# Performance work log

Measured on AMD Instinct MI355X. Metric: run time of the kernel, lower is better.

Reference implementation:

```python
import jax, jax.numpy as jnp
import numpy as np

B, DIN, D, C = 8192, 1024, 768, 16384

def setup_inputs() -> dict:
    key = jax.random.key(0)
    k1, k2, k3 = jax.random.split(key, 3)
    x = jax.random.normal(k1, (B, DIN), dtype=jnp.float32)
    W = jax.random.normal(k2, (DIN, D), dtype=jnp.float32) * 0.02  # backbone final projection
    centroids = jax.random.normal(k3, (C, D), dtype=jnp.float32)
    return {"x": x, "W": W, "centroids": centroids}

def reference(x, W, centroids):
    # backbone embedding: [B, D]
    e = x @ W
    # -||e - c||^2 via algebraic expansion: ||e||^2 + ||c||^2 - 2 e.c
    # (same math as -((e[:,None]-centroids[None])**2).sum(-1), GEMM-formulated)
    e_sq = jnp.sum(e * e, axis=-1, keepdims=True)          # [B, 1]
    c_sq = jnp.sum(centroids * centroids, axis=-1)         # [C]
    cross = e @ centroids.T                                # [B, C]
    return -(e_sq + c_sq[None, :] - 2.0 * cross)           # [B, C]
```

## Files before the change

### kernel.cpp

```cpp
#include <hip/hip_runtime.h>
#include <hip/hip_bf16.h>
#include <cstdint>
#include <cstddef>

#define BB   8192
#define DIN  1024
#define DD   768
#define CC   16384

typedef __bf16 bf16x8 __attribute__((ext_vector_type(8)));
typedef __bf16 bf16x4 __attribute__((ext_vector_type(4)));
typedef float  floatx4 __attribute__((ext_vector_type(4)));

__device__ __forceinline__ void gload_lds16(const void* g, void* l) {
    __builtin_amdgcn_global_load_lds(
        (const __attribute__((address_space(1))) void*)g,
        (__attribute__((address_space(3))) void*)l,
        16, 0, 0);
}


__global__ __launch_bounds__(256) void f2b_kernel(const float4* __restrict__ in,
                                                  bf16x4* __restrict__ out) {
    size_t i = (size_t)blockIdx.x * 256 + threadIdx.x;
    float4 v = in[i];
    bf16x4 o;
    o.x = (__bf16)v.x; o.y = (__bf16)v.y; o.z = (__bf16)v.z; o.w = (__bf16)v.w;
    out[i] = o;
}

__global__ __launch_bounds__(256) void row_convert_sumsq_f32(const float* __restrict__ src,
                                                             __bf16* __restrict__ dst,
                                                             float* __restrict__ sq,
                                                             int Dd) {
    int row = blockIdx.x;
    int tid = threadIdx.x, lane = tid & 63, wave = tid >> 6;
    const float* s = src + (size_t)row * Dd;
    __bf16* d = dst + (size_t)row * Dd;
    float acc = 0.f;
    for (int j = tid; j < Dd; j += 256) {
        __bf16 b = (__bf16)s[j];
        d[j] = b;
        float f = (float)b;
        acc += f * f;
    }
    for (int off = 32; off > 0; off >>= 1) acc += __shfl_xor(acc, off, 64);
    __shared__ float red[4];
    if (lane == 0) red[wave] = acc;
    __syncthreads();
    if (tid == 0) sq[row] = red[0] + red[1] + red[2] + red[3];
}

__global__ __launch_bounds__(256) void row_sumsq_bf16(const __bf16* __restrict__ src,
                                                      float* __restrict__ sq,
                                                      int Dd) {
    int row = blockIdx.x;
    int tid = threadIdx.x, lane = tid & 63, wave = tid >> 6;
    const __bf16* s = src + (size_t)row * Dd;
    float acc = 0.f;
    for (int j = tid; j < Dd; j += 256) {
        float f = (float)s[j];
        acc += f * f;
    }
    for (int off = 32; off > 0; off >>= 1) acc += __shfl_xor(acc, off, 64);
    __shared__ float red[4];
    if (lane == 0) red[wave] = acc;
    __syncthreads();
    if (tid == 0) sq[row] = red[0] + red[1] + red[2] + red[3];
}

__global__ __launch_bounds__(256) void transpose_w(const float* __restrict__ W,
                                                   __bf16* __restrict__ Wt,
                                                   int K, int N) {
    __shared__ float tile[32][33];
    int bx = blockIdx.x * 32;
    int by = blockIdx.y * 32;
    int tx = threadIdx.x & 31, ty = threadIdx.x >> 5;
    for (int i = 0; i < 32; i += 8)
        tile[ty + i][tx] = W[(size_t)(by + ty + i) * N + bx + tx];
    __syncthreads();
    for (int i = 0; i < 32; i += 8)
        Wt[(size_t)(bx + ty + i) * K + by + tx] = (__bf16)tile[tx][ty + i];
}

template <int EPI>
__global__ __launch_bounds__(256) void gemm_bt(const __bf16* __restrict__ A,
                                               const __bf16* __restrict__ Bt,
                                               void* __restrict__ OutP,
                                               const float* __restrict__ esq,
                                               const float* __restrict__ csq,
                                               int M, int N, int K) {
    __shared__ __bf16 As[128 * 64];
    __shared__ __bf16 Bs[128 * 64];
    const int tid  = threadIdx.x;
    const int lane = tid & 63;
    const int wave = tid >> 6;
    const int bm = blockIdx.x * 128;
    const int bn = blockIdx.y * 128;

    floatx4 acc[4][4] = {};

    const int srow = lane >> 3;
    const int sk   = (lane & 7) * 8;

    const int wm   = (wave & 1) * 64;
    const int wn   = (wave >> 1) * 64;
    const int frow = lane & 15;
    const int fk   = (lane >> 4) * 8;

    for (int k0 = 0; k0 < K; k0 += 64) {
        __syncthreads();
        #pragma unroll
        for (int i = 0; i < 4; ++i) {
            int row = wave * 32 + i * 8;
            const __bf16* ga = A  + (size_t)(bm + row + srow) * K + k0 + sk;
            gload_lds16(ga, &As[(size_t)row * 64]);
            const __bf16* gb = Bt + (size_t)(bn + row + srow) * K + k0 + sk;
            gload_lds16(gb, &Bs[(size_t)row * 64]);
        }
        asm volatile("s_waitcnt vmcnt(0)" ::: "memory");
        __syncthreads();

        #pragma unroll
        for (int kk = 0; kk < 64; kk += 32) {
            bf16x8 af[4], bfr[4];
            #pragma unroll
            for (int mi = 0; mi < 4; ++mi)
                af[mi] = *(const bf16x8*)&As[(wm + mi * 16 + frow) * 64 + kk + fk];
            #pragma unroll
            for (int ni = 0; ni < 4; ++ni)
                bfr[ni] = *(const bf16x8*)&Bs[(wn + ni * 16 + frow) * 64 + kk + fk];
            #pragma unroll
            for (int mi = 0; mi < 4; ++mi)
                #pragma unroll
                for (int ni = 0; ni < 4; ++ni)
                    acc[mi][ni] = __builtin_amdgcn_mfma_f32_16x16x32_bf16(
                        af[mi], bfr[ni], acc[mi][ni], 0, 0, 0);
        }
    }

    const int colw = lane & 15;
    const int rowq = (lane >> 4) * 4;
    if (EPI == 1) {
        float* Out = (float*)OutP;
        #pragma unroll
        for (int mi = 0; mi < 4; ++mi) {
            #pragma unroll
            for (int ni = 0; ni < 4; ++ni) {
                int col = bn + wn + ni * 16 + colw;
                float cs = csq[col];
                #pragma unroll
                for (int r = 0; r < 4; ++r) {
                    int row = bm + wm + mi * 16 + rowq + r;
                    Out[(size_t)row * N + col] = 2.0f * acc[mi][ni][r] - esq[row] - cs;
                }
            }
        }
    } else {
        __bf16* Out = (__bf16*)OutP;
        #pragma unroll
        for (int mi = 0; mi < 4; ++mi) {
            #pragma unroll
            for (int ni = 0; ni < 4; ++ni) {
                int col = bn + wn + ni * 16 + colw;
                #pragma unroll
                for (int r = 0; r < 4; ++r) {
                    int row = bm + wm + mi * 16 + rowq + r;
                    Out[(size_t)row * N + col] = (__bf16)acc[mi][ni][r];
                }
            }
        }
    }
}


extern "C" void kernel_launch(void* const* d_in, const int* in_sizes, int n_in,
                              void* d_out, int out_size, void* d_ws, size_t ws_size,
                              hipStream_t stream) {
    const float* x    = (const float*)d_in[0];
    const float* W    = (const float*)d_in[1];
    const float* cent = (const float*)d_in[2];
    float* out = (float*)d_out;

    char* ws = (char*)d_ws;
    __bf16* xb  = (__bf16*)ws;  ws += (size_t)BB * DIN * 2;
    __bf16* Wt  = (__bf16*)ws;  ws += (size_t)DD * DIN * 2;
    __bf16* cb  = (__bf16*)ws;  ws += (size_t)CC * DD * 2;
    float*  csq = (float*)ws;   ws += (size_t)CC * 4;
    __bf16* eb  = (__bf16*)ws;  ws += (size_t)BB * DD * 2;
    float*  esq = (float*)ws;   ws += (size_t)BB * 4;

    f2b_kernel<<<(BB * DIN) / (256 * 4), 256, 0, stream>>>((const float4*)x, (bf16x4*)xb);
    transpose_w<<<dim3(DD / 32, DIN / 32), 256, 0, stream>>>(W, Wt, DIN, DD);
    row_convert_sumsq_f32<<<CC, 256, 0, stream>>>(cent, cb, csq, DD);
    gemm_bt<0><<<dim3(BB / 128, DD / 128), 256, 0, stream>>>(xb, Wt, eb, nullptr, nullptr,
                                                             BB, DD, DIN);
    row_sumsq_bf16<<<BB, 256, 0, stream>>>(eb, esq, DD);
    gemm_bt<1><<<dim3(BB / 128, CC / 128), 256, 0, stream>>>(eb, cb, out, esq, csq,
                                                             BB, CC, DD);
}
```

Baseline: 935.9 us.

## Swizzle LDS tiles, remap blocks per XCD, vectorize epilogue with nontemporal stores

Applies an XOR swizzle to the LDS column chunks on both the global-to-LDS load and the fragment reads, to avoid LDS bank conflicts. Remaps the 1D grid so each XCD works on a fixed band of centroid columns, aiming for better L2 reuse of the B operand. The MFMA operands are swapped so each lane holds four consecutive columns, which lets the epilogue emit vectorized float4 nontemporal stores and bf16x4 stores. The XCD mapping hardcodes the grid shape (128 column tiles, 8 XCDs) and depends on round-robin dispatch of blocks to XCDs.

```diff
diff --git a/kernel.cpp b/kernel.cpp
--- a/kernel.cpp
+++ b/kernel.cpp
@@ -83,7 +83,7 @@
         Wt[(size_t)(bx + ty + i) * K + by + tx] = (__bf16)tile[tx][ty + i];
 }
 
-template <int EPI>
+template <int EPI, int SWIZ>
 __global__ __launch_bounds__(256) void gemm_bt(const __bf16* __restrict__ A,
                                                const __bf16* __restrict__ Bt,
                                                void* __restrict__ OutP,
@@ -95,79 +95,100 @@
     const int tid  = threadIdx.x;
     const int lane = tid & 63;
     const int wave = tid >> 6;
-    const int bm = blockIdx.x * 128;
-    const int bn = blockIdx.y * 128;
+
+    int bm, bn;
+    if (SWIZ == 1) {
+        int flat = blockIdx.x;
+        int xcd = flat & 7;
+        int j = flat >> 3;
+        bn = (xcd * 16 + (j & 15)) * 128;
+        bm = (j >> 4) * 128;
+    } else {
+        int flat = blockIdx.x;
+        int nt = N / 128;
+        bm = (flat / nt) * 128;
+        bn = (flat % nt) * 128;
+    }
 
     floatx4 acc[4][4] = {};
 
     const int srow = lane >> 3;
-    const int sk   = (lane & 7) * 8;
+    const int sc   = ((lane & 7) ^ srow) * 8;
 
     const int wm   = (wave & 1) * 64;
     const int wn   = (wave >> 1) * 64;
     const int frow = lane & 15;
-    const int fk   = (lane >> 4) * 8;
+    const int quad = lane >> 4;
+    const int swz  = frow & 7;
 
     for (int k0 = 0; k0 < K; k0 += 64) {
         __syncthreads();
         #pragma unroll
         for (int i = 0; i < 4; ++i) {
             int row = wave * 32 + i * 8;
-            const __bf16* ga = A  + (size_t)(bm + row + srow) * K + k0 + sk;
+            const __bf16* ga = A  + (size_t)(bm + row + srow) * K + k0 + sc;
             gload_lds16(ga, &As[(size_t)row * 64]);
-            const __bf16* gb = Bt + (size_t)(bn + row + srow) * K + k0 + sk;
+            const __bf16* gb = Bt + (size_t)(bn + row + srow) * K + k0 + sc;
             gload_lds16(gb, &Bs[(size_t)row * 64]);
         }
         asm volatile("s_waitcnt vmcnt(0)" ::: "memory");
         __syncthreads();
 
         #pragma unroll
-        for (int kk = 0; kk < 64; kk += 32) {
+        for (int kb = 0; kb < 2; ++kb) {
             bf16x8 af[4], bfr[4];
             #pragma unroll
             for (int mi = 0; mi < 4; ++mi)
-                af[mi] = *(const bf16x8*)&As[(wm + mi * 16 + frow) * 64 + kk + fk];
+                af[mi] = *(const bf16x8*)&As[(wm + mi * 16 + frow) * 64 +
+                                             (((kb * 4 + quad) ^ swz) * 8)];
             #pragma unroll
             for (int ni = 0; ni < 4; ++ni)
-                bfr[ni] = *(const bf16x8*)&Bs[(wn + ni * 16 + frow) * 64 + kk + fk];
+                bfr[ni] = *(const bf16x8*)&Bs[(wn + ni * 16 + frow) * 64 +
+                                              (((kb * 4 + quad) ^ swz) * 8)];
             #pragma unroll
             for (int mi = 0; mi < 4; ++mi)
                 #pragma unroll
                 for (int ni = 0; ni < 4; ++ni)
                     acc[mi][ni] = __builtin_amdgcn_mfma_f32_16x16x32_bf16(
-                        af[mi], bfr[ni], acc[mi][ni], 0, 0, 0);
-        }
-    }
-
-    const int colw = lane & 15;
-    const int rowq = (lane >> 4) * 4;
+                        bfr[ni], af[mi], acc[mi][ni], 0, 0, 0);
+        }
+    }
+
+    const int mrow = lane & 15;
+    const int nq   = (lane >> 4) * 4;
     if (EPI == 1) {
         float* Out = (float*)OutP;
         #pragma unroll
         for (int mi = 0; mi < 4; ++mi) {
+            int row = bm + wm + mi * 16 + mrow;
+            float es = esq[row];
+            size_t rb = (size_t)row * N;
             #pragma unroll
             for (int ni = 0; ni < 4; ++ni) {
-                int col = bn + wn + ni * 16 + colw;
-                float cs = csq[col];
+                int col = bn + wn + ni * 16 + nq;
+                floatx4 cs = *(const floatx4*)&csq[col];
+                floatx4 a = acc[mi][ni];
+                floatx4 v;
                 #pragma unroll
-                for (int r = 0; r < 4; ++r) {
-                    int row = bm + wm + mi * 16 + rowq + r;
-                    Out[(size_t)row * N + col] = 2.0f * acc[mi][ni][r] - esq[row] - cs;
-                }
+                for (int r = 0; r < 4; ++r)
+                    v[r] = 2.0f * a[r] - es - cs[r];
+                __builtin_nontemporal_store(v, (floatx4*)&Out[rb + col]);
             }
         }
     } else {
         __bf16* Out = (__bf16*)OutP;
         #pragma unroll
         for (int mi = 0; mi < 4; ++mi) {
+            int row = bm + wm + mi * 16 + mrow;
+            size_t rb = (size_t)row * N;
             #pragma unroll
             for (int ni = 0; ni < 4; ++ni) {
-                int col = bn + wn + ni * 16 + colw;
+                int col = bn + wn + ni * 16 + nq;
+                floatx4 a = acc[mi][ni];
+                bf16x4 o;
                 #pragma unroll
-                for (int r = 0; r < 4; ++r) {
-                    int row = bm + wm + mi * 16 + rowq + r;
-                    Out[(size_t)row * N + col] = (__bf16)acc[mi][ni][r];
-                }
+                for (int r = 0; r < 4; ++r) o[r] = (__bf16)a[r];
+                *(bf16x4*)&Out[rb + col] = o;
             }
         }
     }
@@ -193,9 +214,9 @@
     f2b_kernel<<<(BB * DIN) / (256 * 4), 256, 0, stream>>>((const float4*)x, (bf16x4*)xb);
     transpose_w<<<dim3(DD / 32, DIN / 32), 256, 0, stream>>>(W, Wt, DIN, DD);
     row_convert_sumsq_f32<<<CC, 256, 0, stream>>>(cent, cb, csq, DD);
-    gemm_bt<0><<<dim3(BB / 128, DD / 128), 256, 0, stream>>>(xb, Wt, eb, nullptr, nullptr,
-                                                             BB, DD, DIN);
+    gemm_bt<0, 0><<<(BB / 128) * (DD / 128), 256, 0, stream>>>(xb, Wt, eb, nullptr, nullptr,
+                                                               BB, DD, DIN);
     row_sumsq_bf16<<<BB, 256, 0, stream>>>(eb, esq, DD);
-    gemm_bt<1><<<dim3(BB / 128, CC / 128), 256, 0, stream>>>(eb, cb, out, esq, csq,
-                                                             BB, CC, DD);
-}
+    gemm_bt<1, 1><<<(BB / 128) * (CC / 128), 256, 0, stream>>>(eb, cb, out, esq, csq,
+                                                               BB, CC, DD);
+}
```

New measurement: 830.1 us. -11.3%, faster.
